# Kernel optimization log

Hardware: AMD Instinct MI355X
Metric: run time of the kernel (lower is better)

Reference implementation:

```python
import jax, jax.numpy as jnp
import numpy as np


def setup_inputs() -> dict:
    key = jax.random.key(0)
    k1, k2 = jax.random.split(key, 2)
    N, C, H, W, G = 64, 256, 56, 56, 32
    x = jax.random.normal(k1, (N, C, H, W), dtype=jnp.float32)
    # fc: Linear(batch_size*2 -> group)
    fc_w = jax.random.normal(k2, (G, 2 * N), dtype=jnp.float32) * 0.05
    fc_b = jnp.zeros((G,), dtype=jnp.float32)
    # affine params (1, C, 1, 1), init ones/zeros as in the module
    weight = jnp.ones((1, C, 1, 1), dtype=jnp.float32)
    bias = jnp.zeros((1, C, 1, 1), dtype=jnp.float32)
    return {"x": x, "fc_w": fc_w, "fc_b": fc_b, "weight": weight, "bias": bias, "group": G}


def reference(x, fc_w, fc_b, weight, bias, group):
    eps = 1e-5
    N, C, H, W = x.shape
    hw = H * W
    # --- routing features: per-channel mean/var over (N is kept, reduce HW) ---
    # torch: x_ = x.transpose(0,1).view(C,N,HW); mean/var(-1) with unbiased var (ddof=1)
    mean_cn = jnp.mean(x, axis=(2, 3)).T           # [C, N]
    var_cn = jnp.var(x, axis=(2, 3), ddof=1).T     # [C, N]
    s = jnp.concatenate([mean_cn, var_cn], axis=1)  # [C, 2N]
    probs = jax.nn.softmax(s @ fc_w.T + fc_b, axis=1)  # [C, G]
    g = jnp.argmax(probs, axis=1)                  # [C] channel -> group
    onehot = jax.nn.one_hot(g, group, dtype=x.dtype)  # [C, G]
    # --- per-(sample, group) mean/var via segment reduce expressed as GEMM ---
    s1 = jnp.sum(x, axis=(2, 3))        # [N, C]
    s2 = jnp.sum(x * x, axis=(2, 3))    # [N, C]
    S1 = s1 @ onehot                    # [N, G]
    S2 = s2 @ onehot                    # [N, G]
    cnt = jnp.sum(onehot, axis=0) * hw  # [G] elements per (n, g)
    mean_g = S1 / jnp.maximum(cnt, 1.0)                          # [N, G]
    # unbiased variance (torch .var default): (sum_sq - n*mean^2)/(n-1)
    var_g = (S2 - S1 * mean_g) / jnp.maximum(cnt - 1.0, 1.0)     # [N, G]
    # empty groups are skipped in the original; no channel maps to them, so
    # the guarded denominators only prevent NaNs and never affect outputs.
    mean_c = mean_g[:, g]  # [N, C] gather per-channel stats
    var_c = var_g[:, g]    # [N, C]
    xn = (x - mean_c[:, :, None, None]) * jax.lax.rsqrt(var_c + eps)[:, :, None, None]
    return xn * weight + bias
```

## Files before the change

kernel.cpp:

```cpp
#include <hip/hip_runtime.h>

constexpr int N_  = 64;
constexpr int C_  = 256;
constexpr int HW_ = 56 * 56;
constexpr int G_  = 32;
constexpr int NC_ = N_ * C_;
constexpr float EPS_ = 1e-5f;

__global__ __launch_bounds__(256) void k_sums(const float* __restrict__ x,
                                              float* __restrict__ s1,
                                              float* __restrict__ s2) {
    const int nc = blockIdx.x;
    const float4* xp = reinterpret_cast<const float4*>(x + (size_t)nc * HW_);
    constexpr int NV = HW_ / 4;
    float a = 0.f, b = 0.f;
    for (int i = threadIdx.x; i < NV; i += 256) {
        float4 v = xp[i];
        a += v.x + v.y + v.z + v.w;
        b += v.x * v.x + v.y * v.y + v.z * v.z + v.w * v.w;
    }
    for (int off = 32; off; off >>= 1) {
        a += __shfl_down(a, off, 64);
        b += __shfl_down(b, off, 64);
    }
    __shared__ float sa[4], sb[4];
    const int wid = threadIdx.x >> 6, lane = threadIdx.x & 63;
    if (lane == 0) { sa[wid] = a; sb[wid] = b; }
    __syncthreads();
    if (threadIdx.x == 0) {
        s1[nc] = sa[0] + sa[1] + sa[2] + sa[3];
        s2[nc] = sb[0] + sb[1] + sb[2] + sb[3];
    }
}

__global__ __launch_bounds__(64) void k_logits(const float* __restrict__ s1,
                                               const float* __restrict__ s2,
                                               const float* __restrict__ fc_w,
                                               const float* __restrict__ fc_b,
                                               int* __restrict__ gidx) {
    const int c = blockIdx.x;
    const int t = threadIdx.x;
    const int g = t & 31, half = t >> 5;
    const float inv_hw  = 1.f / (float)HW_;
    const float inv_hw1 = 1.f / (float)(HW_ - 1);
    const float* wg = fc_w + g * (2 * N_);
    float acc = half ? 0.f : fc_b[g];
    const int n0 = half * 32;
    #pragma unroll 8
    for (int n = n0; n < n0 + 32; ++n) {
        const float v1 = s1[n * C_ + c];
        const float v2 = s2[n * C_ + c];
        const float m  = v1 * inv_hw;
        const float vr = (v2 - v1 * m) * inv_hw1;
        acc += m * wg[n] + vr * wg[N_ + n];
    }
    acc += __shfl_down(acc, 32, 64);
    __shared__ float lg[G_];
    if (half == 0) lg[g] = acc;
    __syncthreads();
    if (t == 0) {
        float best = lg[0];
        int bi = 0;
        for (int g2 = 1; g2 < G_; ++g2) {
            const float v = lg[g2];
            if (v > best) { best = v; bi = g2; }
        }
        gidx[c] = bi;
    }
}

__global__ __launch_bounds__(256) void k_group(const float* __restrict__ s1,
                                               const float* __restrict__ s2,
                                               const int* __restrict__ gidx,
                                               const float* __restrict__ weight,
                                               const float* __restrict__ bias,
                                               float* __restrict__ scale,
                                               float* __restrict__ shift) {
    const int n = blockIdx.x;
    const int c = threadIdx.x;
    __shared__ float r1[C_], r2[C_];
    __shared__ int   gi[C_];
    __shared__ float mg[G_], ig[G_];
    r1[c] = s1[n * C_ + c];
    r2[c] = s2[n * C_ + c];
    gi[c] = gidx[c];
    __syncthreads();
    if (c < G_) {
        float A = 0.f, B = 0.f;
        int k = 0;
        for (int cc = 0; cc < C_; ++cc) {
            if (gi[cc] == c) { A += r1[cc]; B += r2[cc]; ++k; }
        }
        const float cf = (float)k * (float)HW_;
        const float m  = A / fmaxf(cf, 1.f);
        const float vr = (B - A * m) / fmaxf(cf - 1.f, 1.f);
        mg[c] = m;
        ig[c] = rsqrtf(vr + EPS_);
    }
    __syncthreads();
    const int g = gi[c];
    const float sc = ig[g] * weight[c];
    scale[n * C_ + c] = sc;
    shift[n * C_ + c] = bias[c] - mg[g] * sc;
}

__global__ __launch_bounds__(256) void k_norm(const float* __restrict__ x,
                                              const float* __restrict__ scale,
                                              const float* __restrict__ shift,
                                              float* __restrict__ out) {
    const int nc = blockIdx.x;
    const float sc = scale[nc];
    const float sh = shift[nc];
    const float4* xp = reinterpret_cast<const float4*>(x + (size_t)nc * HW_);
    float4* op = reinterpret_cast<float4*>(out + (size_t)nc * HW_);
    constexpr int NV = HW_ / 4;
    for (int i = threadIdx.x; i < NV; i += 256) {
        float4 v = xp[i];
        v.x = v.x * sc + sh;
        v.y = v.y * sc + sh;
        v.z = v.z * sc + sh;
        v.w = v.w * sc + sh;
        op[i] = v;
    }
}

extern "C" void kernel_launch(void* const* d_in, const int* in_sizes, int n_in,
                              void* d_out, int out_size, void* d_ws, size_t ws_size,
                              hipStream_t stream) {
    const float* x      = (const float*)d_in[0];
    const float* fc_w   = (const float*)d_in[1];
    const float* fc_b   = (const float*)d_in[2];
    const float* weight = (const float*)d_in[3];
    const float* bias   = (const float*)d_in[4];
    float* out = (float*)d_out;

    float* ws    = (float*)d_ws;
    float* s1    = ws;
    float* s2    = ws + NC_;
    float* scale = ws + 2 * NC_;
    float* shift = ws + 3 * NC_;
    int*   gidx  = (int*)(ws + 4 * NC_);

    k_sums  <<<NC_, 256, 0, stream>>>(x, s1, s2);
    k_logits<<<C_,   64, 0, stream>>>(s1, s2, fc_w, fc_b, gidx);
    k_group <<<N_,  256, 0, stream>>>(s1, s2, gidx, weight, bias, scale, shift);
    k_norm  <<<NC_, 256, 0, stream>>>(x, scale, shift, out);
}
```

Before: 133.7 us.

## Assign one wave per channel row with fully unrolled loads and nontemporal stores

Both the reduction and normalize kernels now give each 64-lane wave its own (n,c) row instead of spreading one row across a 256-thread block. Each lane issues all 12 vector loads up front, plus a 16-lane tail, so more memory requests are in flight at once. The block-level shared-memory reduction and its barrier are gone, since a single wave shuffle now covers the row. Output is written with nontemporal stores to avoid polluting the cache, at the cost of more registers per thread.

```diff
diff --git a/kernel.cpp b/kernel.cpp
--- a/kernel.cpp
+++ b/kernel.cpp
@@ -7,30 +7,37 @@
 constexpr int NC_ = N_ * C_;
 constexpr float EPS_ = 1e-5f;
 
+typedef float f32x4 __attribute__((ext_vector_type(4)));
+
 __global__ __launch_bounds__(256) void k_sums(const float* __restrict__ x,
                                               float* __restrict__ s1,
                                               float* __restrict__ s2) {
-    const int nc = blockIdx.x;
-    const float4* xp = reinterpret_cast<const float4*>(x + (size_t)nc * HW_);
-    constexpr int NV = HW_ / 4;
+    const int wave = threadIdx.x >> 6;
+    const int lane = threadIdx.x & 63;
+    const int nc = blockIdx.x * 4 + wave;
+    const f32x4* xp = reinterpret_cast<const f32x4*>(x + (size_t)nc * HW_);
+    f32x4 v[12];
+    #pragma unroll
+    for (int k = 0; k < 12; ++k) v[k] = xp[lane + k * 64];
+    f32x4 vt;
+    const bool tail = lane < 16;
+    if (tail) vt = xp[768 + lane];
     float a = 0.f, b = 0.f;
-    for (int i = threadIdx.x; i < NV; i += 256) {
-        float4 v = xp[i];
-        a += v.x + v.y + v.z + v.w;
-        b += v.x * v.x + v.y * v.y + v.z * v.z + v.w * v.w;
+    #pragma unroll
+    for (int k = 0; k < 12; ++k) {
+        a += (v[k].x + v[k].y) + (v[k].z + v[k].w);
+        b += (v[k].x * v[k].x + v[k].y * v[k].y) + (v[k].z * v[k].z + v[k].w * v[k].w);
     }
+    if (tail) {
+        a += (vt.x + vt.y) + (vt.z + vt.w);
+        b += (vt.x * vt.x + vt.y * vt.y) + (vt.z * vt.z + vt.w * vt.w);
+    }
+    #pragma unroll
     for (int off = 32; off; off >>= 1) {
         a += __shfl_down(a, off, 64);
         b += __shfl_down(b, off, 64);
     }
-    __shared__ float sa[4], sb[4];
-    const int wid = threadIdx.x >> 6, lane = threadIdx.x & 63;
-    if (lane == 0) { sa[wid] = a; sb[wid] = b; }
-    __syncthreads();
-    if (threadIdx.x == 0) {
-        s1[nc] = sa[0] + sa[1] + sa[2] + sa[3];
-        s2[nc] = sb[0] + sb[1] + sb[2] + sb[3];
-    }
+    if (lane == 0) { s1[nc] = a; s2[nc] = b; }
 }
 
 __global__ __launch_bounds__(64) void k_logits(const float* __restrict__ s1,
@@ -108,19 +115,27 @@
                                               const float* __restrict__ scale,
                                               const float* __restrict__ shift,
                                               float* __restrict__ out) {
-    const int nc = blockIdx.x;
+    const int wave = threadIdx.x >> 6;
+    const int lane = threadIdx.x & 63;
+    const int nc = blockIdx.x * 4 + wave;
     const float sc = scale[nc];
     const float sh = shift[nc];
-    const float4* xp = reinterpret_cast<const float4*>(x + (size_t)nc * HW_);
-    float4* op = reinterpret_cast<float4*>(out + (size_t)nc * HW_);
-    constexpr int NV = HW_ / 4;
-    for (int i = threadIdx.x; i < NV; i += 256) {
-        float4 v = xp[i];
-        v.x = v.x * sc + sh;
-        v.y = v.y * sc + sh;
-        v.z = v.z * sc + sh;
-        v.w = v.w * sc + sh;
-        op[i] = v;
+    const f32x4* xp = reinterpret_cast<const f32x4*>(x + (size_t)nc * HW_);
+    f32x4* op = reinterpret_cast<f32x4*>(out + (size_t)nc * HW_);
+    f32x4 v[12];
+    #pragma unroll
+    for (int k = 0; k < 12; ++k) v[k] = xp[lane + k * 64];
+    f32x4 vt;
+    const bool tail = lane < 16;
+    if (tail) vt = xp[768 + lane];
+    #pragma unroll
+    for (int k = 0; k < 12; ++k) {
+        v[k] = v[k] * sc + sh;
+        __builtin_nontemporal_store(v[k], op + lane + k * 64);
+    }
+    if (tail) {
+        vt = vt * sc + sh;
+        __builtin_nontemporal_store(vt, op + 768 + lane);
     }
 }
 
@@ -141,8 +156,8 @@
     float* shift = ws + 3 * NC_;
     int*   gidx  = (int*)(ws + 4 * NC_);
 
-    k_sums  <<<NC_, 256, 0, stream>>>(x, s1, s2);
-    k_logits<<<C_,   64, 0, stream>>>(s1, s2, fc_w, fc_b, gidx);
-    k_group <<<N_,  256, 0, stream>>>(s1, s2, gidx, weight, bias, scale, shift);
-    k_norm  <<<NC_, 256, 0, stream>>>(x, scale, shift, out);
+    k_sums  <<<NC_ / 4, 256, 0, stream>>>(x, s1, s2);
+    k_logits<<<C_,       64, 0, stream>>>(s1, s2, fc_w, fc_b, gidx);
+    k_group <<<N_,      256, 0, stream>>>(s1, s2, gidx, weight, bias, scale, shift);
+    k_norm  <<<NC_ / 4, 256, 0, stream>>>(x, scale, shift, out);
 }
```

Result: faster. 120.6 us (-9.8%).
